# Kernel optimization log

Hardware: AMD Instinct MI355X
Metric: run time of the kernel (lower is better)

Reference implementation:

```python
import jax, jax.numpy as jnp
import numpy as np

# ---- constants matching init_kwargs ----
NX = NY = 4096
DX = DY = 1.0
DT = 0.1
CX = CY = 1.0
OMEGA = 1.0
NLEVEL = int(np.log2(min(NX, NY) / 128)) + 1  # 6 levels
DIAG = 1.0 + CX * DT / DX + CY * DT / DY       # removed diagonal of stencil

# 3x3 upwind stencil with diagonal zeroed (as in the torch module)
_A_np = np.zeros((1, 1, 3, 3), np.float32)
_A_np[0, 0, 1, 0] = -CX * DT / DX
_A_np[0, 0, 0, 1] = -CY * DT / DY
A_SMOOTH = jnp.asarray(_A_np)
# 2x2 restriction kernel (average), stride 2
A_RES = jnp.full((1, 1, 2, 2), 0.25, jnp.float32)


def _conv(x, k, stride):
    return jax.lax.conv_general_dilated(
        x, k, window_strides=(stride, stride), padding='VALID',
        dimension_numbers=('NCHW', 'OIHW', 'NCHW'))


def _bc(u):
    # replicate edges into a 1-cell halo, corners stay zero (exactly as torch code)
    ny, nx = u.shape[2], u.shape[3]
    p = jnp.zeros((1, 1, ny + 2, nx + 2), u.dtype)
    p = p.at[0, 0, 1:-1, 1:-1].set(u[0, 0])
    p = p.at[0, 0, -1, 1:-1].set(u[0, 0, -1, :])
    p = p.at[0, 0, 0, 1:-1].set(u[0, 0, 0, :])
    p = p.at[0, 0, 1:-1, -1].set(u[0, 0, :, -1])
    p = p.at[0, 0, 1:-1, 0].set(u[0, 0, :, 0])
    return p


def _prol(x):
    return jnp.repeat(jnp.repeat(x, 2, axis=2), 2, axis=3)


def _f_cycle(u, b_smooth, b_res, t):
    smooth = lambda x: _conv(x, A_SMOOTH, 1) + b_smooth  # bias broadcasts over HW
    res = lambda x: _conv(x, A_RES, 2) + b_res
    for _ in range(t):
        # source term b = 0 in the original module
        r = smooth(_bc(u))                                   # (1,1,NY,NX)
        r_s = [r]
        for _i in range(1, NLEVEL):
            r = res(r)                                       # halve resolution
            r_s.append(r)
        e = jnp.zeros((1, 1, 1, 1), u.dtype)
        for j in reversed(range(1, NLEVEL)):
            e_pad = jnp.pad(e, ((0, 0), (0, 0), (1, 1), (1, 1)))
            e = e - smooth(e_pad) / DIAG + r_s[j] / DIAG      # broadcasts on 1st step
            e = _prol(e)
        u_update = u - e - smooth(_bc(u)) / DIAG
        u = (1.0 - OMEGA) * u + OMEGA * u_update
    return u


def setup_inputs() -> dict:
    key = jax.random.key(0)
    k1, k2, k3 = jax.random.split(key, 3)
    u = jax.random.normal(k1, (1, 1, NY, NX), dtype=jnp.float32)
    b_smooth = jax.random.normal(k2, (1,), dtype=jnp.float32)
    b_res = jax.random.normal(k3, (1,), dtype=jnp.float32)
    return {"u": u, "b_smooth": b_smooth, "b_res": b_res, "t": 4}


def reference(u, b_smooth, b_res, t):
    return _f_cycle(u, b_smooth, b_res, t)
```

## Files before the change

kernel.cpp:

```cpp
#include <hip/hip_runtime.h>

#define NXY 4096

constexpr float DT_DX    = 0.1f;
constexpr float INV_DIAG = 1.0f / 1.2f;

__global__ __launch_bounds__(256, 8) void k_fcycle(
    const float* __restrict__ u,
    const float* __restrict__ bsp, const float* __restrict__ brp,
    float* __restrict__ uo)
{
    __shared__ float sr2[24][40];
    __shared__ float sr3[12][20];
    __shared__ float sr4[6][10];
    __shared__ float se5[3][5];
    __shared__ float se4[5][9];
    __shared__ float se3[9][17];
    __shared__ float se2[17][33];

    const float bs = bsp[0];
    const float br = brp[0];
    const int tid = threadIdx.x;

    const int bid = blockIdx.x;
    const int swz = (bid & 7) * 256 + (bid >> 3);
    const int by = swz >> 5, bx = swz & 31;

    const int Ax = bx * 64, Ay = by * 32;
    const int Ux = Ax * 2, Uy = Ay * 2;
    const bool leftB = (bx == 0);

    {
        const int l = tid & 63;
        const int s = tid >> 6;
        if (l < 40) {
            const int rc0 = Ux - 32 + 4 * l;
            const int c4  = max(rc0, 0) >> 2;
            const int ry0 = Uy - 32 + 24 * s;
            auto ld = [&](int k) -> float4 {
                return ((const float4*)(u + max(ry0 + k, 0) * NXY))[c4];
            };
            float ecol = 0.f;
            if (!leftB && l < 24) ecol = u[max(ry0 + l, 0) * NXY + (Ux - 33)];
            float4 vup = ld(-1);
            float4 q0 = ld(0), q1 = ld(1), q2 = ld(2), q3 = ld(3), q4 = ld(4);
            float h0p = 0.f, h1p = 0.f, aP = 0.f, bP = 0.f;
            #pragma unroll
            for (int k = 0; k < 24; ++k) {
                float4 vc;
                switch (k % 5) {
                    case 0: vc = q0; if (k + 5 < 24) q0 = ld(k + 5); break;
                    case 1: vc = q1; if (k + 5 < 24) q1 = ld(k + 5); break;
                    case 2: vc = q2; if (k + 5 < 24) q2 = ld(k + 5); break;
                    case 3: vc = q3; if (k + 5 < 24) q3 = ld(k + 5); break;
                    default: vc = q4; if (k + 5 < 24) q4 = ld(k + 5); break;
                }
                const float lwS = __shfl_up(vc.w, 1);
                const float lwE = __shfl(ecol, k);
                const float lw  = leftB ? ((l <= 8) ? vc.x : lwS)
                                        : (l ? lwS : lwE);
                const float rx  = -DT_DX * (lw   + vup.x) + bs;
                const float ry_ = -DT_DX * (vc.x + vup.y) + bs;
                const float rz  = -DT_DX * (vc.y + vup.z) + bs;
                const float rw  = -DT_DX * (vc.z + vup.w) + bs;
                const float h0 = rx + ry_, h1 = rz + rw;
                if ((k & 1) == 0) { h0p = h0; h1p = h1; }
                else {
                    const float a = 0.25f * (h0p + h0) + br;
                    const float b = 0.25f * (h1p + h1) + br;
                    if ((k & 3) == 1) { aP = a; bP = b; }
                    else sr2[6 * s + (k >> 2)][l] = 0.25f * (aP + bP + a + b) + br;
                }
                vup = vc;
            }
        }
    }

    const int lane = tid & 31;
    const int tyf  = tid >> 5;
    const int gx4  = (Ux >> 2) + lane;
    const int gy0  = Uy + tyf * 8;
    auto ldI = [&](int k) -> float4 {
        return ((const float4*)(u + (gy0 + k) * NXY))[gx4];
    };
    float ecolI = 0.f;
    if (!leftB && lane < 8) ecolI = u[(gy0 + lane) * NXY + (Ux - 1)];
    float4 vupI = ((const float4*)(u + (gy0 ? gy0 - 1 : 0) * NXY))[gx4];
    float4 p0 = ldI(0), p1 = ldI(1), p2 = ldI(2), p3 = ldI(3);

    __syncthreads();

    if (tid < 240) {
        const int Y = tid / 20, X = tid - Y * 20;
        sr3[Y][X] = 0.25f * (sr2[2*Y][2*X] + sr2[2*Y][2*X+1] +
                             sr2[2*Y+1][2*X] + sr2[2*Y+1][2*X+1]) + br;
    }
    __syncthreads();

    if (tid < 64) {
        if (tid < 60) {
            const int Y = tid / 10, X = tid - Y * 10;
            sr4[Y][X] = 0.25f * (sr3[2*Y][2*X] + sr3[2*Y][2*X+1] +
                                 sr3[2*Y+1][2*X] + sr3[2*Y+1][2*X+1]) + br;
        }
        if (tid < 15) {
            const int Y = tid / 5, X = tid - Y * 5;
            const int gy = 2 * by - 1 + Y, gx = 4 * bx - 1 + X;
            const float r5 = 0.25f * (sr4[2*Y][2*X] + sr4[2*Y][2*X+1] +
                                      sr4[2*Y+1][2*X] + sr4[2*Y+1][2*X+1]) + br;
            se5[Y][X] = (gy >= 0 && gx >= 0) ? (r5 - bs) * INV_DIAG : 0.f;
        }
        if (tid < 45) {
            const int r = tid / 9, c = tid - r * 9;
            const int gy = 4 * by - 1 + r, gx = 8 * bx - 1 + c;
            float v = 0.f;
            if (gy >= 0 && gx >= 0) {
                const int l5y = 2 * by - 1, l5x = 4 * bx - 1;
                const float P  = se5[(gy >> 1) - l5y][(gx >> 1) - l5x];
                const float Pu = gy ? se5[((gy - 1) >> 1) - l5y][(gx >> 1) - l5x] : 0.f;
                const float Pl = gx ? se5[(gy >> 1) - l5y][((gx - 1) >> 1) - l5x] : 0.f;
                v = P + (DT_DX * (Pl + Pu) - bs + sr4[r + 1][c + 1]) * INV_DIAG;
            }
            se4[r][c] = v;
        }
    }
    __syncthreads();

    if (tid < 153) {
        const int r = tid / 17, c = tid - r * 17;
        const int gy = 8 * by - 1 + r, gx = 16 * bx - 1 + c;
        float v = 0.f;
        if (gy >= 0 && gx >= 0) {
            const int l4y = 4 * by - 1, l4x = 8 * bx - 1;
            const float P  = se4[(gy >> 1) - l4y][(gx >> 1) - l4x];
            const float Pu = gy ? se4[((gy - 1) >> 1) - l4y][(gx >> 1) - l4x] : 0.f;
            const float Pl = gx ? se4[(gy >> 1) - l4y][((gx - 1) >> 1) - l4x] : 0.f;
            v = P + (DT_DX * (Pl + Pu) - bs + sr3[r + 3][c + 3]) * INV_DIAG;
        }
        se3[r][c] = v;
    }
    __syncthreads();

    for (int i = tid; i < 561; i += 256) {
        const int r = i / 33, c = i - r * 33;
        const int gy = 16 * by - 1 + r, gx = 32 * bx - 1 + c;
        float v = 0.f;
        if (gy >= 0 && gx >= 0) {
            const int l3y = 8 * by - 1, l3x = 16 * bx - 1;
            const float P  = se3[(gy >> 1) - l3y][(gx >> 1) - l3x];
            const float Pu = gy ? se3[((gy - 1) >> 1) - l3y][(gx >> 1) - l3x] : 0.f;
            const float Pl = gx ? se3[(gy >> 1) - l3y][((gx - 1) >> 1) - l3x] : 0.f;
            v = P + (DT_DX * (Pl + Pu) - bs + sr2[r + 7][c + 7]) * INV_DIAG;
        }
        se2[r][c] = v;
    }
    __syncthreads();

    const int l2y = 16 * by - 1;
    float4 vup = vupI;
    float rxE = 0.f, ryE = 0.f, rzE = 0.f, rwE = 0.f;
    float4 vcE = make_float4(0.f, 0.f, 0.f, 0.f);
    #pragma unroll
    for (int k = 0; k < 8; ++k) {
        float4 vc;
        switch (k & 3) {
            case 0: vc = p0; if (k + 4 < 8) p0 = ldI(k + 4); break;
            case 1: vc = p1; if (k + 4 < 8) p1 = ldI(k + 4); break;
            case 2: vc = p2; if (k + 4 < 8) p2 = ldI(k + 4); break;
            default: vc = p3; if (k + 4 < 8) p3 = ldI(k + 4); break;
        }
        const int gy = gy0 + k;
        const float lwS = __shfl_up(vc.w, 1, 32);
        const float lwE = __shfl(ecolI, (tid & 32) + k);
        const float lw  = leftB ? (lane ? lwS : vc.x)
                                : (lane ? lwS : lwE);
        const float rx  = -DT_DX * (lw   + vup.x) + bs;
        const float ry_ = -DT_DX * (vc.x + vup.y) + bs;
        const float rz  = -DT_DX * (vc.y + vup.z) + bs;
        const float rw  = -DT_DX * (vc.z + vup.w) + bs;
        if ((k & 1) == 0) { rxE = rx; ryE = ry_; rzE = rz; rwE = rw; vcE = vc; }
        else {
            const float r10 = 0.25f * (rxE + ryE + rx + ry_) + br;
            const float r11 = 0.25f * (rzE + rwE + rz + rw) + br;
            const int E  = (gy - 1) >> 1;
            const int pr = (E >> 1) - l2y;
            const int pc = lane + 1;
            const float P0  = se2[pr][pc];
            const float Pu0 = E ? se2[((E - 1) >> 1) - l2y][pc] : 0.f;
            const int  C0 = Ax + 2 * lane;
            const float Pl0 = C0 ? se2[pr][pc - 1] : 0.f;
            const float ex = P0 + (DT_DX * (Pl0 + Pu0) - bs + r10) * INV_DIAG;
            const float ey = P0 + (DT_DX * (P0  + Pu0) - bs + r11) * INV_DIAG;
            float4 oE, o;
            oE.x = vcE.x - ex - rxE * INV_DIAG;
            oE.y = vcE.y - ex - ryE * INV_DIAG;
            oE.z = vcE.z - ey - rzE * INV_DIAG;
            oE.w = vcE.w - ey - rwE * INV_DIAG;
            o.x  = vc.x  - ex - rx  * INV_DIAG;
            o.y  = vc.y  - ex - ry_ * INV_DIAG;
            o.z  = vc.z  - ey - rz  * INV_DIAG;
            o.w  = vc.w  - ey - rw  * INV_DIAG;
            ((float4*)(uo + (gy - 1) * NXY))[gx4] = oE;
            ((float4*)(uo + gy * NXY))[gx4] = o;
        }
        vup = vc;
    }
}

extern "C" void kernel_launch(void* const* d_in, const int* in_sizes, int n_in,
                              void* d_out, int out_size, void* d_ws, size_t ws_size,
                              hipStream_t stream)
{
    const float* u_in = (const float*)d_in[0];
    const float* bs   = (const float*)d_in[1];
    const float* br   = (const float*)d_in[2];
    float* out = (float*)d_out;
    float* w0  = (float*)d_ws;

    const float* src = u_in;
    for (int it = 0; it < 4; ++it) {
        float* dst = (it & 1) ? out : w0;
        k_fcycle<<<2048, 256, 0, stream>>>(src, bs, br, dst);
        src = dst;
    }
}
```

Baseline: 120.4 us.

## Deepen load prefetch and merge coarse-level phases into one wavefront

The halo restriction loop now keeps eight rows of float4 loads in flight instead of five. The interior tile prefetches all eight rows before the coarse-level work, so none of those loads wait behind it. The sr3, sr4/se5/se4 and se3 phases now run inside the first 64 threads, which removes two block-wide barriers because a single wavefront runs them in lockstep. This raises register pressure under launch_bounds(256,8), which could cause spills. It also serialises the sr3 and se3 work onto one wave, which may lengthen the critical path.

```diff
diff --git a/kernel.cpp b/kernel.cpp
--- a/kernel.cpp
+++ b/kernel.cpp
@@ -43,17 +43,21 @@
             float ecol = 0.f;
             if (!leftB && l < 24) ecol = u[max(ry0 + l, 0) * NXY + (Ux - 33)];
             float4 vup = ld(-1);
-            float4 q0 = ld(0), q1 = ld(1), q2 = ld(2), q3 = ld(3), q4 = ld(4);
+            float4 q0 = ld(0), q1 = ld(1), q2 = ld(2), q3 = ld(3);
+            float4 q4 = ld(4), q5 = ld(5), q6 = ld(6), q7 = ld(7);
             float h0p = 0.f, h1p = 0.f, aP = 0.f, bP = 0.f;
             #pragma unroll
             for (int k = 0; k < 24; ++k) {
                 float4 vc;
-                switch (k % 5) {
-                    case 0: vc = q0; if (k + 5 < 24) q0 = ld(k + 5); break;
-                    case 1: vc = q1; if (k + 5 < 24) q1 = ld(k + 5); break;
-                    case 2: vc = q2; if (k + 5 < 24) q2 = ld(k + 5); break;
-                    case 3: vc = q3; if (k + 5 < 24) q3 = ld(k + 5); break;
-                    default: vc = q4; if (k + 5 < 24) q4 = ld(k + 5); break;
+                switch (k & 7) {
+                    case 0: vc = q0; if (k + 8 < 24) q0 = ld(k + 8); break;
+                    case 1: vc = q1; if (k + 8 < 24) q1 = ld(k + 8); break;
+                    case 2: vc = q2; if (k + 8 < 24) q2 = ld(k + 8); break;
+                    case 3: vc = q3; if (k + 8 < 24) q3 = ld(k + 8); break;
+                    case 4: vc = q4; if (k + 8 < 24) q4 = ld(k + 8); break;
+                    case 5: vc = q5; if (k + 8 < 24) q5 = ld(k + 8); break;
+                    case 6: vc = q6; if (k + 8 < 24) q6 = ld(k + 8); break;
+                    default: vc = q7; if (k + 8 < 24) q7 = ld(k + 8); break;
                 }
                 const float lwS = __shfl_up(vc.w, 1);
                 const float lwE = __shfl(ecol, k);
@@ -87,17 +91,16 @@
     if (!leftB && lane < 8) ecolI = u[(gy0 + lane) * NXY + (Ux - 1)];
     float4 vupI = ((const float4*)(u + (gy0 ? gy0 - 1 : 0) * NXY))[gx4];
     float4 p0 = ldI(0), p1 = ldI(1), p2 = ldI(2), p3 = ldI(3);
+    float4 p4 = ldI(4), p5 = ldI(5), p6 = ldI(6), p7 = ldI(7);
 
     __syncthreads();
 
-    if (tid < 240) {
-        const int Y = tid / 20, X = tid - Y * 20;
-        sr3[Y][X] = 0.25f * (sr2[2*Y][2*X] + sr2[2*Y][2*X+1] +
-                             sr2[2*Y+1][2*X] + sr2[2*Y+1][2*X+1]) + br;
-    }
-    __syncthreads();
-
     if (tid < 64) {
+        for (int i = tid; i < 240; i += 64) {
+            const int Y = i / 20, X = i - Y * 20;
+            sr3[Y][X] = 0.25f * (sr2[2*Y][2*X] + sr2[2*Y][2*X+1] +
+                                 sr2[2*Y+1][2*X] + sr2[2*Y+1][2*X+1]) + br;
+        }
         if (tid < 60) {
             const int Y = tid / 10, X = tid - Y * 10;
             sr4[Y][X] = 0.25f * (sr3[2*Y][2*X] + sr3[2*Y][2*X+1] +
@@ -123,21 +126,19 @@
             }
             se4[r][c] = v;
         }
-    }
-    __syncthreads();
-
-    if (tid < 153) {
-        const int r = tid / 17, c = tid - r * 17;
-        const int gy = 8 * by - 1 + r, gx = 16 * bx - 1 + c;
-        float v = 0.f;
-        if (gy >= 0 && gx >= 0) {
-            const int l4y = 4 * by - 1, l4x = 8 * bx - 1;
-            const float P  = se4[(gy >> 1) - l4y][(gx >> 1) - l4x];
-            const float Pu = gy ? se4[((gy - 1) >> 1) - l4y][(gx >> 1) - l4x] : 0.f;
-            const float Pl = gx ? se4[(gy >> 1) - l4y][((gx - 1) >> 1) - l4x] : 0.f;
-            v = P + (DT_DX * (Pl + Pu) - bs + sr3[r + 3][c + 3]) * INV_DIAG;
-        }
-        se3[r][c] = v;
+        for (int i = tid; i < 153; i += 64) {
+            const int r = i / 17, c = i - r * 17;
+            const int gy = 8 * by - 1 + r, gx = 16 * bx - 1 + c;
+            float v = 0.f;
+            if (gy >= 0 && gx >= 0) {
+                const int l4y = 4 * by - 1, l4x = 8 * bx - 1;
+                const float P  = se4[(gy >> 1) - l4y][(gx >> 1) - l4x];
+                const float Pu = gy ? se4[((gy - 1) >> 1) - l4y][(gx >> 1) - l4x] : 0.f;
+                const float Pl = gx ? se4[(gy >> 1) - l4y][((gx - 1) >> 1) - l4x] : 0.f;
+                v = P + (DT_DX * (Pl + Pu) - bs + sr3[r + 3][c + 3]) * INV_DIAG;
+            }
+            se3[r][c] = v;
+        }
     }
     __syncthreads();
 
@@ -163,11 +164,15 @@
     #pragma unroll
     for (int k = 0; k < 8; ++k) {
         float4 vc;
-        switch (k & 3) {
-            case 0: vc = p0; if (k + 4 < 8) p0 = ldI(k + 4); break;
-            case 1: vc = p1; if (k + 4 < 8) p1 = ldI(k + 4); break;
-            case 2: vc = p2; if (k + 4 < 8) p2 = ldI(k + 4); break;
-            default: vc = p3; if (k + 4 < 8) p3 = ldI(k + 4); break;
+        switch (k) {
+            case 0: vc = p0; break;
+            case 1: vc = p1; break;
+            case 2: vc = p2; break;
+            case 3: vc = p3; break;
+            case 4: vc = p4; break;
+            case 5: vc = p5; break;
+            case 6: vc = p6; break;
+            default: vc = p7; break;
         }
         const int gy = gy0 + k;
         const float lwS = __shfl_up(vc.w, 1, 32);
```

New measurement: 115.6 us. 4.0% less time.
